# Optimization experiments

Measured on AMD Instinct MI355X. Metric: run time of the kernel, lower is better.

The kernel has to match this reference:

```python
import jax, jax.numpy as jnp
from jax import lax
import numpy as np

B, T, D, H = 512, 512, 128, 64


def setup_inputs() -> dict:
    key = jax.random.key(0)
    k_x, k_wi, k_wh, k_bi, k_bh = jax.random.split(key, 5)
    s = 1.0 / np.sqrt(H)  # torch LSTM init scale
    return {
        "x": jax.random.normal(k_x, (B, T, D), dtype=jnp.float32),
        "W_ih": jax.random.uniform(k_wi, (4 * H, D), minval=-s, maxval=s, dtype=jnp.float32),
        "W_hh": jax.random.uniform(k_wh, (4 * H, H), minval=-s, maxval=s, dtype=jnp.float32),
        "b_ih": jax.random.uniform(k_bi, (4 * H,), minval=-s, maxval=s, dtype=jnp.float32),
        "b_hh": jax.random.uniform(k_bh, (4 * H,), minval=-s, maxval=s, dtype=jnp.float32),
    }


def reference(x, W_ih, W_hh, b_ih, b_hh):
    # x: [B, T, D]; torch LSTM gate order: i, f, g, o
    Bv, Tv, _ = x.shape
    Hv = W_hh.shape[1]
    # Precompute all input-to-gate projections in one big GEMM: [B, T, 4H]
    xg = jnp.einsum("btd,gd->btg", x, W_ih) + b_ih + b_hh
    xg_t = jnp.swapaxes(xg, 0, 1)  # [T, B, 4H] for scan over time

    def step(carry, xt):
        h, c = carry
        gates = xt + h @ W_hh.T  # [B, 4H]
        i, f, g, o = jnp.split(gates, 4, axis=-1)
        i = jax.nn.sigmoid(i)
        f = jax.nn.sigmoid(f)
        g = jnp.tanh(g)
        o = jax.nn.sigmoid(o)
        c = f * c + i * g
        h = o * jnp.tanh(c)
        return (h, c), None

    h0 = jnp.zeros((Bv, Hv), dtype=x.dtype)
    (h_last, _), _ = lax.scan(step, (h0, h0), xg_t)
    return h_last  # out[:, -1, :] == final hidden state of a single-layer LSTM
```

## Files before the change

kernel.cpp:

```cpp
#include <hip/hip_runtime.h>
#include <hip/hip_fp16.h>
#include <math.h>


#define Bsz   512
#define Tlen  512
#define Din   128
#define Hdim  64
#define NGATE 256

typedef __attribute__((ext_vector_type(8))) short short8v;
typedef __attribute__((ext_vector_type(4))) float f32x4;
typedef __attribute__((ext_vector_type(2))) _Float16 h2v;
typedef unsigned short ushort_t;
typedef unsigned int uint_t;
typedef __attribute__((ext_vector_type(4))) uint_t uint4v;

__device__ __forceinline__ unsigned short f2bf_bits(float f) {
    union { float f; unsigned u; } v; v.f = f;
    unsigned r = v.u + 0x7fff + ((v.u >> 16) & 1);
    return (unsigned short)(r >> 16);
}
__device__ __forceinline__ float bf2f(unsigned short b) {
    union { unsigned u; float f; } v; v.u = ((unsigned)b) << 16;
    return v.f;
}
__device__ __forceinline__ uint_t pkh(float a, float b) {
    return (uint_t)__half_as_ushort(__float2half(a)) |
           ((uint_t)__half_as_ushort(__float2half(b)) << 16);
}
__device__ __forceinline__ h2v as_h2(uint_t u) {
    union { uint_t u; h2v h; } v; v.u = u; return v.h;
}
__device__ __forceinline__ float f16lo(uint_t u) {
    return __half2float(__ushort_as_half((ushort_t)(u & 0xffff)));
}
__device__ __forceinline__ float f16hi(uint_t u) {
    return __half2float(__ushort_as_half((ushort_t)(u >> 16)));
}
__device__ __forceinline__ float sigmoid_f(float v) {
    return 1.0f / (1.0f + __expf(-v));
}
__device__ __forceinline__ float tanh_f(float v) {
    float a = fabsf(v);
    float e = __expf(2.0f * a);
    float r = 1.0f - 2.0f / (e + 1.0f);
    return copysignf(r, v);
}

#if defined(__has_builtin)
#if __has_builtin(__builtin_amdgcn_fdot2)
#define FDOT2(a, b, c) __builtin_amdgcn_fdot2((a), (b), (c), false)
#endif
#endif
#ifndef FDOT2
#define FDOT2(a, b, c) fmaf((float)(a)[1], (float)(b)[1], fmaf((float)(a)[0], (float)(b)[0], (c)))
#endif

#define MF(acc, a, b) acc = __builtin_amdgcn_mfma_f32_16x16x32_bf16(a, b, acc, 0, 0, 0)

__global__ __launch_bounds__(256, 1)
void xg_gemm2(const float* __restrict__ x, const float* __restrict__ W_ih,
              const float* __restrict__ b_ih, const float* __restrict__ b_hh,
              uint_t* __restrict__ xg)
{
    __shared__ __align__(16) ushort_t sxh[2][16][136];
    __shared__ __align__(16) ushort_t sxl[2][16][136];

    const int tid = threadIdx.x;
    const int l = tid & 63, q = tid >> 6;
    const int jl = l & 15, s4 = l >> 4;
    const int rb = blockIdx.x & 31, tc = blockIdx.x >> 5;
    const int t0 = tc * 32;

    short8v wb[4][4];
    #pragma unroll
    for (int tt = 0; tt < 4; ++tt) {
        #pragma unroll
        for (int kt = 0; kt < 4; ++kt) {
            const float* wp = W_ih + (size_t)(tt * 64 + q * 16 + jl) * Din + kt * 32 + s4 * 8;
            f32x4 v0 = *(const f32x4*)wp;
            f32x4 v1 = *(const f32x4*)(wp + 4);
            #pragma unroll
            for (int j = 0; j < 8; ++j)
                wb[tt][kt][j] = (short)f2bf_bits((j < 4) ? v0[j] : v1[j - 4]);
        }
    }
    float bias[4];
    #pragma unroll
    for (int tt = 0; tt < 4; ++tt) {
        int g = tt * 64 + q * 16 + jl;
        bias[tt] = b_ih[g] + b_hh[g];
    }

    const int srow = tid >> 4, spart = tid & 15;
    const float* xrow = x + (size_t)(rb * 16 + srow) * Tlen * Din + spart * 8;
    f32x4 xr0 = *(const f32x4*)(xrow + (size_t)t0 * Din);
    f32x4 xr1 = *(const f32x4*)(xrow + (size_t)t0 * Din + 4);

    for (int ti = 0; ti < 32; ++ti) {
        const int t = t0 + ti, buf = ti & 1;

        short8v vh, vl;
        #pragma unroll
        for (int j = 0; j < 8; ++j) {
            float f = (j < 4) ? xr0[j] : xr1[j - 4];
            unsigned short hb = f2bf_bits(f);
            vh[j] = (short)hb;
            vl[j] = (short)f2bf_bits(f - bf2f(hb));
        }
        *(short8v*)&sxh[buf][srow][spart * 8] = vh;
        *(short8v*)&sxl[buf][srow][spart * 8] = vl;
        __syncthreads();

        if (ti + 1 < 32) {
            xr0 = *(const f32x4*)(xrow + (size_t)(t + 1) * Din);
            xr1 = *(const f32x4*)(xrow + (size_t)(t + 1) * Din + 4);
        }

        f32x4 acc0 = {0.f, 0.f, 0.f, 0.f}, acc1 = acc0, acc2 = acc0, acc3 = acc0;
        #pragma unroll
        for (int kt = 0; kt < 4; ++kt) {
            short8v ah = *(const short8v*)&sxh[buf][jl][kt * 32 + s4 * 8];
            short8v al = *(const short8v*)&sxl[buf][jl][kt * 32 + s4 * 8];
            MF(acc0, ah, wb[0][kt]); MF(acc1, ah, wb[1][kt]);
            MF(acc2, ah, wb[2][kt]); MF(acc3, ah, wb[3][kt]);
            MF(acc0, al, wb[0][kt]); MF(acc1, al, wb[1][kt]);
            MF(acc2, al, wb[2][kt]); MF(acc3, al, wb[3][kt]);
        }

        #pragma unroll
        for (int r = 0; r < 4; ++r) {
            const int brow = rb * 16 + s4 * 4 + r;
            uint2 st;
            st.x = pkh(acc0[r] + bias[0], acc1[r] + bias[1]);
            st.y = pkh(acc2[r] + bias[2], acc3[r] + bias[3]);
            *(uint2*)(xg + ((size_t)brow * Tlen + t) * 128 + (q * 16 + jl) * 2) = st;
        }
    }
}

__global__ __launch_bounds__(256, 1)
void lstm_rec8(const uint_t* __restrict__ xg, const float* __restrict__ W_hh,
               float* __restrict__ out)
{
    __shared__ float    gsh[2][4][Hdim];
    __shared__ __align__(16) ushort_t hsh[4][Hdim];

    const int tid = threadIdx.x;
    const int j  = tid & 63;
    const int tt = tid >> 6;

    uint4v Wq[8];
    {
        const float2* wr = (const float2*)(W_hh + (size_t)(tt * Hdim + j) * Hdim);
        #pragma unroll
        for (int qq = 0; qq < 8; ++qq) {
            #pragma unroll
            for (int cc = 0; cc < 4; ++cc) {
                float2 w = wr[qq * 4 + cc];
                Wq[qq][cc] = pkh(w.x, w.y);
            }
        }
    }

    hsh[tt][j] = 0;
    asm volatile("" ::: "memory");
    float c = 0.0f, h = 0.0f;

    const int b = blockIdx.x;
    const uint_t* xp = xg + (size_t)b * (Tlen * 128) + j * 2 + (tt >> 1);

    uint_t xA[16], xB[16];
    #pragma unroll
    for (int i = 0; i < 16; ++i) xA[i] = xp[(size_t)i * 128];
    #pragma unroll
    for (int i = 0; i < 16; ++i) xB[i] = xp[(size_t)(16 + i) * 128];

    const uint4v* hp = (const uint4v*)&hsh[tt][0];

#define STEP1(xv, SI) do {                                                     \
    uint4v hq[8];                                                              \
    _Pragma("unroll")                                                          \
    for (int i_ = 0; i_ < 8; ++i_) hq[i_] = hp[i_];                            \
    float a0 = (tt & 1) ? f16hi(xv) : f16lo(xv);                               \
    float a1 = 0.f, a2 = 0.f, a3 = 0.f;                                        \
    _Pragma("unroll")                                                          \
    for (int qq = 0; qq < 8; ++qq) {                                           \
        a0 = FDOT2(as_h2(hq[qq][0]), as_h2(Wq[qq][0]), a0);                    \
        a1 = FDOT2(as_h2(hq[qq][1]), as_h2(Wq[qq][1]), a1);                    \
        a2 = FDOT2(as_h2(hq[qq][2]), as_h2(Wq[qq][2]), a2);                    \
        a3 = FDOT2(as_h2(hq[qq][3]), as_h2(Wq[qq][3]), a3);                    \
    }                                                                          \
    float pre = (a0 + a1) + (a2 + a3);                                         \
    float act = (tt == 2) ? tanh_f(pre) : sigmoid_f(pre);                      \
    gsh[(SI) & 1][tt][j] = act;                                                \
    __syncthreads();                                                           \
    float iv = gsh[(SI) & 1][0][j];                                            \
    float fv = gsh[(SI) & 1][1][j];                                            \
    float gv = gsh[(SI) & 1][2][j];                                            \
    float ov = gsh[(SI) & 1][3][j];                                            \
    c = fv * c + iv * gv;                                                      \
    h = ov * tanh_f(c);                                                        \
    hsh[tt][j] = __half_as_ushort(__float2half(h));                            \
    asm volatile("" ::: "memory");                                             \
} while (0)

#define STEP16(XARR) do {                                                      \
    _Pragma("unroll")                                                          \
    for (int si_ = 0; si_ < 16; ++si_) STEP1(XARR[si_], si_);                  \
} while (0)

    for (int bt = 0; bt < 32; bt += 2) {
        STEP16(xA);
        if (bt + 2 < 32) {
            const uint_t* rp = xp + (size_t)(bt + 2) * 16 * 128;
            #pragma unroll
            for (int i = 0; i < 16; ++i) xA[i] = rp[(size_t)i * 128];
        }
        STEP16(xB);
        if (bt + 3 < 32) {
            const uint_t* rp = xp + (size_t)(bt + 3) * 16 * 128;
            #pragma unroll
            for (int i = 0; i < 16; ++i) xB[i] = rp[(size_t)i * 128];
        }
    }
#undef STEP16
#undef STEP1

    if (tt == 0) out[(size_t)b * Hdim + j] = h;
}

#define LDS_DWORDS 33920
__global__ void __launch_bounds__(256, 1)
lstm_fused(const float* __restrict__ x, const float* __restrict__ W_ih,
           const float* __restrict__ W_hh, const float* __restrict__ b_ih,
           const float* __restrict__ b_hh, float* __restrict__ out)
{
    extern __shared__ float lds[];
    float* wih   = lds;
    float* xbuf  = lds + 32768;
    float* gates = lds + 33280;
    float* hbuf  = lds + 33792;

    const int tid = threadIdx.x;
    const int g   = tid;
    const int row_base = blockIdx.x * 2;

    {
        const float4* src = reinterpret_cast<const float4*>(W_ih);
        float4* dst = reinterpret_cast<float4*>(wih);
        #pragma unroll
        for (int i = 0; i < 32; ++i) {
            int qq = i * 256 + tid;
            int rg = qq >> 5;
            int cc = qq & 31;
            dst[rg * 32 + (cc ^ (rg & 7))] = src[qq];
        }
    }
    float4 whh[16];
    {
        const float4* src = reinterpret_cast<const float4*>(W_hh) + g * 16;
        #pragma unroll
        for (int cc = 0; cc < 16; ++cc) whh[cc] = src[cc];
    }
    const float bias = b_ih[g] + b_hh[g];
    if (tid < 128) hbuf[tid] = 0.0f;
    {
        int r = tid >> 7, k = tid & 127;
        xbuf[tid] = x[((size_t)(row_base + r) * Tlen + 0) * Din + k];
    }
    float cstate = 0.0f, hval = 0.0f;
    __syncthreads();

    int cur = 0;
    const int sw = g & 7;
    const float4* w4 = reinterpret_cast<const float4*>(wih) + g * 32;

    for (int t = 0; t < Tlen; ++t) {
        float xnext = 0.0f;
        if (t + 1 < Tlen) {
            int r = tid >> 7, k = tid & 127;
            xnext = x[((size_t)(row_base + r) * Tlen + (t + 1)) * Din + k];
        }
        float acc0 = bias, acc1 = bias;
        {
            const float4* xr0 = reinterpret_cast<const float4*>(xbuf + cur * 256);
            const float4* xr1 = reinterpret_cast<const float4*>(xbuf + cur * 256 + 128);
            #pragma unroll 8
            for (int cc = 0; cc < 32; ++cc) {
                float4 w = w4[cc ^ sw];
                float4 a = xr0[cc];
                float4 bb = xr1[cc];
                acc0 += w.x * a.x + w.y * a.y + w.z * a.z + w.w * a.w;
                acc1 += w.x * bb.x + w.y * bb.y + w.z * bb.z + w.w * bb.w;
            }
        }
        {
            const float4* h0 = reinterpret_cast<const float4*>(hbuf);
            const float4* h1 = reinterpret_cast<const float4*>(hbuf + 64);
            #pragma unroll
            for (int cc = 0; cc < 16; ++cc) {
                float4 w = whh[cc];
                float4 a = h0[cc];
                float4 bb = h1[cc];
                acc0 += w.x * a.x + w.y * a.y + w.z * a.z + w.w * a.w;
                acc1 += w.x * bb.x + w.y * bb.y + w.z * bb.z + w.w * bb.w;
            }
        }
        gates[g]       = acc0;
        gates[256 + g] = acc1;
        __syncthreads();

        if (tid < 128) {
            int r = tid >> 6, jj = tid & 63;
            const float* gr = gates + r * 256;
            float ig = sigmoid_f(gr[jj]);
            float fg = sigmoid_f(gr[64 + jj]);
            float gg = tanh_f(gr[128 + jj]);
            float og = sigmoid_f(gr[192 + jj]);
            cstate = fg * cstate + ig * gg;
            hval   = og * tanh_f(cstate);
            hbuf[r * 64 + jj] = hval;
        }
        if (t + 1 < Tlen) xbuf[(cur ^ 1) * 256 + tid] = xnext;
        __syncthreads();
        cur ^= 1;
    }
    if (tid < 128) {
        int r = tid >> 6, jj = tid & 63;
        out[(size_t)(row_base + r) * Hdim + jj] = hval;
    }
}

extern "C" void kernel_launch(void* const* d_in, const int* in_sizes, int n_in,
                              void* d_out, int out_size, void* d_ws, size_t ws_size,
                              hipStream_t stream) {
    const float* x    = (const float*)d_in[0];
    const float* W_ih = (const float*)d_in[1];
    const float* W_hh = (const float*)d_in[2];
    const float* b_ih = (const float*)d_in[3];
    const float* b_hh = (const float*)d_in[4];
    float* out = (float*)d_out;

    const size_t need = (size_t)Bsz * Tlen * NGATE * 2;
    if (ws_size >= need) {
        uint_t* xgws = (uint_t*)d_ws;
        xg_gemm2<<<512, 256, 0, stream>>>(x, W_ih, b_ih, b_hh, xgws);
        lstm_rec8<<<Bsz, 256, 0, stream>>>(xgws, W_hh, out);
    } else {
        const size_t lds_bytes = (size_t)LDS_DWORDS * 4;
        hipFuncSetAttribute(reinterpret_cast<const void*>(lstm_fused),
                            hipFuncAttributeMaxDynamicSharedMemorySize, (int)lds_bytes);
        lstm_fused<<<Bsz / 2, 256, lds_bytes, stream>>>(x, W_ih, W_hh, b_ih, b_hh, out);
    }
}
```

Before: 307.6 us.

## Halve recurrent block to two waves, each computing two gates per hidden unit

The recurrent kernel now runs each batch row with 128 threads (two wavefronts) instead of 256. Each thread keeps two rows of W_hh in registers and computes two gate pre-activations per step, sharing the h loads across both. Gate activations are exchanged as a float2 between the two waves, and the h buffer is double-buffered to avoid a write-after-read hazard. This cuts barrier participants and LDS traffic per step, and lets more blocks fit per CU. In exchange each thread does twice the serial dot-product work, and register pressure rises.

Result: slower. 396.1 us (+28.8%).

```diff
diff --git a/kernel.cpp b/kernel.cpp
--- a/kernel.cpp
+++ b/kernel.cpp
@@ -140,95 +140,106 @@
     }
 }
 
-__global__ __launch_bounds__(256, 1)
-void lstm_rec8(const uint_t* __restrict__ xg, const float* __restrict__ W_hh,
-               float* __restrict__ out)
+__global__ __launch_bounds__(128, 1)
+void lstm_rec10(const uint_t* __restrict__ xg, const float* __restrict__ W_hh,
+                float* __restrict__ out)
 {
-    __shared__ float    gsh[2][4][Hdim];
-    __shared__ __align__(16) ushort_t hsh[4][Hdim];
+    __shared__ float2 gx[2][2][Hdim];
+    __shared__ __align__(16) ushort_t hsh[2][2][Hdim];
 
     const int tid = threadIdx.x;
-    const int j  = tid & 63;
-    const int tt = tid >> 6;
-
-    uint4v Wq[8];
+    const int j = tid & 63;
+    const int p = tid >> 6;
+    const int b = blockIdx.x;
+
+    uint4v WA[8], WB[8];
     {
-        const float2* wr = (const float2*)(W_hh + (size_t)(tt * Hdim + j) * Hdim);
+        const float2* wra = (const float2*)(W_hh + (size_t)((2 * p) * Hdim + j) * Hdim);
+        const float2* wrb = (const float2*)(W_hh + (size_t)((2 * p + 1) * Hdim + j) * Hdim);
         #pragma unroll
         for (int qq = 0; qq < 8; ++qq) {
             #pragma unroll
             for (int cc = 0; cc < 4; ++cc) {
-                float2 w = wr[qq * 4 + cc];
-                Wq[qq][cc] = pkh(w.x, w.y);
+                float2 wa = wra[qq * 4 + cc];
+                float2 wb2 = wrb[qq * 4 + cc];
+                WA[qq][cc] = pkh(wa.x, wa.y);
+                WB[qq][cc] = pkh(wb2.x, wb2.y);
             }
         }
     }
 
-    hsh[tt][j] = 0;
+    hsh[p][0][j] = 0;
     asm volatile("" ::: "memory");
     float c = 0.0f, h = 0.0f;
 
-    const int b = blockIdx.x;
-    const uint_t* xp = xg + (size_t)b * (Tlen * 128) + j * 2 + (tt >> 1);
-
-    uint_t xA[16], xB[16];
+    const uint_t* xp = xg + (size_t)b * (Tlen * 128) + j * 2 + p;
+
+    uint_t xA[8], xB[8];
     #pragma unroll
-    for (int i = 0; i < 16; ++i) xA[i] = xp[(size_t)i * 128];
+    for (int i = 0; i < 8; ++i) xA[i] = xp[(size_t)i * 128];
     #pragma unroll
-    for (int i = 0; i < 16; ++i) xB[i] = xp[(size_t)(16 + i) * 128];
-
-    const uint4v* hp = (const uint4v*)&hsh[tt][0];
+    for (int i = 0; i < 8; ++i) xB[i] = xp[(size_t)(8 + i) * 128];
 
 #define STEP1(xv, SI) do {                                                     \
-    uint4v hq[8];                                                              \
+    const int buf_ = (SI) & 1;                                                 \
+    const uint4v* hp_ = (const uint4v*)&hsh[p][buf_][0];                       \
+    uint4v hq_[8];                                                             \
     _Pragma("unroll")                                                          \
-    for (int i_ = 0; i_ < 8; ++i_) hq[i_] = hp[i_];                            \
-    float a0 = (tt & 1) ? f16hi(xv) : f16lo(xv);                               \
-    float a1 = 0.f, a2 = 0.f, a3 = 0.f;                                        \
+    for (int i_ = 0; i_ < 8; ++i_) hq_[i_] = hp_[i_];                          \
+    float a0 = f16lo(xv), b0 = f16hi(xv);                                      \
+    float a1 = 0.f, a2 = 0.f, a3 = 0.f, b1 = 0.f, b2 = 0.f, b3 = 0.f;          \
     _Pragma("unroll")                                                          \
-    for (int qq = 0; qq < 8; ++qq) {                                           \
-        a0 = FDOT2(as_h2(hq[qq][0]), as_h2(Wq[qq][0]), a0);                    \
-        a1 = FDOT2(as_h2(hq[qq][1]), as_h2(Wq[qq][1]), a1);                    \
-        a2 = FDOT2(as_h2(hq[qq][2]), as_h2(Wq[qq][2]), a2);                    \
-        a3 = FDOT2(as_h2(hq[qq][3]), as_h2(Wq[qq][3]), a3);                    \
+    for (int q_ = 0; q_ < 8; ++q_) {                                           \
+        a0 = FDOT2(as_h2(hq_[q_][0]), as_h2(WA[q_][0]), a0);                   \
+        a1 = FDOT2(as_h2(hq_[q_][1]), as_h2(WA[q_][1]), a1);                   \
+        a2 = FDOT2(as_h2(hq_[q_][2]), as_h2(WA[q_][2]), a2);                   \
+        a3 = FDOT2(as_h2(hq_[q_][3]), as_h2(WA[q_][3]), a3);                   \
+        b0 = FDOT2(as_h2(hq_[q_][0]), as_h2(WB[q_][0]), b0);                   \
+        b1 = FDOT2(as_h2(hq_[q_][1]), as_h2(WB[q_][1]), b1);                   \
+        b2 = FDOT2(as_h2(hq_[q_][2]), as_h2(WB[q_][2]), b2);                   \
+        b3 = FDOT2(as_h2(hq_[q_][3]), as_h2(WB[q_][3]), b3);                   \
     }                                                                          \
-    float pre = (a0 + a1) + (a2 + a3);                                         \
-    float act = (tt == 2) ? tanh_f(pre) : sigmoid_f(pre);                      \
-    gsh[(SI) & 1][tt][j] = act;                                                \
+    float preA = (a0 + a1) + (a2 + a3);                                        \
+    float preB = (b0 + b1) + (b2 + b3);                                        \
+    float actB = sigmoid_f(preB);                                  \
+    float actA = p ? tanh_f(preA) : sigmoid_f(preA);               \
+    float2 mine; mine.x = actA; mine.y = actB;                                 \
+    gx[p][buf_][j] = mine;                                                     \
     __syncthreads();                                                           \
-    float iv = gsh[(SI) & 1][0][j];                                            \
-    float fv = gsh[(SI) & 1][1][j];                                            \
-    float gv = gsh[(SI) & 1][2][j];                                            \
-    float ov = gsh[(SI) & 1][3][j];                                            \
+    float2 oth = gx[1 - p][buf_][j];                                           \
+    float iv = p ? oth.x  : actA;                                              \
+    float fv = p ? oth.y  : actB;                                              \
+    float gv = p ? actA   : oth.x;                                             \
+    float ov = p ? actB   : oth.y;                                             \
     c = fv * c + iv * gv;                                                      \
     h = ov * tanh_f(c);                                                        \
-    hsh[tt][j] = __half_as_ushort(__float2half(h));                            \
+    hsh[p][buf_ ^ 1][j] = __half_as_ushort(__float2half(h));                   \
     asm volatile("" ::: "memory");                                             \
 } while (0)
 
-#define STEP16(XARR) do {                                                      \
+#define STEP8(XARR) do {                                                       \
     _Pragma("unroll")                                                          \
-    for (int si_ = 0; si_ < 16; ++si_) STEP1(XARR[si_], si_);                  \
+    for (int si_ = 0; si_ < 8; ++si_) STEP1(XARR[si_], si_);                   \
 } while (0)
 
-    for (int bt = 0; bt < 32; bt += 2) {
-        STEP16(xA);
-        if (bt + 2 < 32) {
-            const uint_t* rp = xp + (size_t)(bt + 2) * 16 * 128;
-            #pragma unroll
-            for (int i = 0; i < 16; ++i) xA[i] = rp[(size_t)i * 128];
-        }
-        STEP16(xB);
-        if (bt + 3 < 32) {
-            const uint_t* rp = xp + (size_t)(bt + 3) * 16 * 128;
-            #pragma unroll
-            for (int i = 0; i < 16; ++i) xB[i] = rp[(size_t)i * 128];
-        }
-    }
-#undef STEP16
+    for (int bt = 0; bt < 64; bt += 2) {
+        STEP8(xA);
+        if (bt + 2 < 64) {
+            const uint_t* rp = xp + (size_t)(bt + 2) * 8 * 128;
+            #pragma unroll
+            for (int i = 0; i < 8; ++i) xA[i] = rp[(size_t)i * 128];
+        }
+        STEP8(xB);
+        if (bt + 3 < 64) {
+            const uint_t* rp = xp + (size_t)(bt + 3) * 8 * 128;
+            #pragma unroll
+            for (int i = 0; i < 8; ++i) xB[i] = rp[(size_t)i * 128];
+        }
+    }
+#undef STEP8
 #undef STEP1
 
-    if (tt == 0) out[(size_t)b * Hdim + j] = h;
+    if (p == 0) out[(size_t)b * Hdim + j] = h;
 }
 
 #define LDS_DWORDS 33920
@@ -347,7 +358,7 @@
     if (ws_size >= need) {
         uint_t* xgws = (uint_t*)d_ws;
         xg_gemm2<<<512, 256, 0, stream>>>(x, W_ih, b_ih, b_hh, xgws);
-        lstm_rec8<<<Bsz, 256, 0, stream>>>(xgws, W_hh, out);
+        lstm_rec10<<<Bsz, 128, 0, stream>>>(xgws, W_hh, out);
     } else {
         const size_t lds_bytes = (size_t)LDS_DWORDS * 4;
         hipFuncSetAttribute(reinterpret_cast<const void*>(lstm_fused),
```
